# Kernel optimization log

Hardware: AMD Instinct MI355X
Metric: run time of the kernel (lower is better)

The kernel has to match this reference:

```python
import jax, jax.numpy as jnp
from jax import lax
import numpy as np

B, T, D = 8, 2048, 1024
EPS = 1e-8


def zc_rms(x, g):
    x0 = x - jnp.mean(x, axis=-1, keepdims=True)
    return x0 * jax.lax.rsqrt(jnp.mean(x0 * x0, axis=-1, keepdims=True) + EPS) * g


def l2norm(x):
    return x * jax.lax.rsqrt(jnp.sum(x * x, axis=-1, keepdims=True) + EPS)


def dwconv3(x, w, b):
    # x: [B, T, D]; w: [D, 3] depthwise kernel; b: [D]
    xc = jnp.transpose(x, (0, 2, 1))  # [B, D, T]
    y = lax.conv_general_dilated(xc, w[:, None, :], window_strides=(1,),
                                 padding=[(1, 1)],
                                 dimension_numbers=('NCH', 'OIH', 'NCH'),
                                 feature_group_count=w.shape[0])
    return jnp.transpose(y + b[:, None], (0, 2, 1))  # [B, T, D]


def setup_inputs() -> dict:
    key = jax.random.key(0)
    ks = jax.random.split(key, 16)
    s = 1.0 / np.sqrt(D)
    inp = {
        'x': jax.random.normal(ks[0], (B, T, D), jnp.float32),
        'g1': jnp.ones((D,), jnp.float32),
        'Wq': jax.random.normal(ks[1], (D, D), jnp.float32) * s,
        'bq': jnp.zeros((D,), jnp.float32),
        'Wk': jax.random.normal(ks[2], (D, D), jnp.float32) * s,
        'bk': jnp.zeros((D,), jnp.float32),
        'Wv': jax.random.normal(ks[3], (D, D), jnp.float32) * s,
        'bv': jnp.zeros((D,), jnp.float32),
        'wqc': jax.random.normal(ks[4], (D, 3), jnp.float32) * 0.5,
        'bqc': jnp.zeros((D,), jnp.float32),
        'wkc': jax.random.normal(ks[5], (D, 3), jnp.float32) * 0.5,
        'bkc': jnp.zeros((D,), jnp.float32),
        'wvc': jax.random.normal(ks[6], (D, 3), jnp.float32) * 0.5,
        'bvc': jnp.zeros((D,), jnp.float32),
        'Wa': jax.random.normal(ks[7], (D, D), jnp.float32) * s,
        'ba': jnp.zeros((D,), jnp.float32),
        'Wb': jax.random.normal(ks[8], (D, D), jnp.float32) * s,
        'bb': jnp.zeros((D,), jnp.float32),
        'g2': jnp.ones((D,), jnp.float32),
        'Wp': jax.random.normal(ks[9], (D, D), jnp.float32) * s,
        'bp': jnp.zeros((D,), jnp.float32),
    }
    return inp


def reference(x, g1, Wq, bq, Wk, bk, Wv, bv, wqc, bqc, wkc, bkc, wvc, bvc,
              Wa, ba, Wb, bb, g2, Wp, bp):
    h = zc_rms(x, g1)
    q = jax.nn.sigmoid(dwconv3(h @ Wq + bq, wqc, bqc))
    k = jax.nn.sigmoid(dwconv3(h @ Wk + bk, wkc, bkc))
    v = jax.nn.sigmoid(dwconv3(h @ Wv + bv, wvc, bvc))
    q, k = l2norm(q), l2norm(k)
    delta = q * (k * v)
    delta = jnp.tanh(x @ Wa + ba) * delta + (x @ Wb + bb)
    dhat = zc_rms(delta, g2) @ Wp + bp
    # dropout is identity in eval mode
    return x + jax.nn.sigmoid(jax.nn.silu(dhat)) * dhat
```

## Files before the change

### kernel.cpp

```cpp
#include <hip/hip_runtime.h>
#include <stdint.h>

#define DD 1024
#define TT 2048
#define BBATCH 8
#define MM (BBATCH*TT)

typedef unsigned short u16;
typedef unsigned int   u32;

typedef __attribute__((ext_vector_type(8))) __bf16 bf16x8;
typedef __attribute__((ext_vector_type(4))) float  floatx4;
typedef __attribute__((ext_vector_type(4))) unsigned short u16x4;
typedef __attribute__((ext_vector_type(8))) unsigned short u16x8;

__device__ __forceinline__ float b2f(u16 v){
    u32 x = ((u32)v) << 16;
    return __builtin_bit_cast(float, x);
}
__device__ __forceinline__ u16 f2b(float f){
    u32 u = __builtin_bit_cast(u32, f);
    u32 r = (u + 0x7fffu + ((u >> 16) & 1u)) >> 16;
    return (u16)r;
}
__device__ __forceinline__ float sigf(float x){
    return 1.0f / (1.0f + __expf(-x));
}
__device__ __forceinline__ float tanhfast(float x){
    float e = __expf(2.0f * x);
    return 1.0f - 2.0f / (e + 1.0f);
}

__device__ __forceinline__ void g2l16(const u16* g, u16* l){
    __builtin_amdgcn_global_load_lds(
        (const __attribute__((address_space(1))) u32*)g,
        (__attribute__((address_space(3))) u32*)l, 16, 0, 0);
}

__device__ __forceinline__ void load4bf(const u16* p, float* o){
    u16x4 v = *(const u16x4*)p;
    o[0] = b2f(v.x); o[1] = b2f(v.y); o[2] = b2f(v.z); o[3] = b2f(v.w);
}

__device__ __forceinline__ void wave_reduce2(float& a, float& b){
    #pragma unroll
    for (int m = 32; m; m >>= 1){
        a += __shfl_xor(a, m, 64);
        b += __shfl_xor(b, m, 64);
    }
}

__device__ __forceinline__ void block_reduce2(float& a, float& b, float* red, int tid){
    #pragma unroll
    for (int off = 32; off; off >>= 1){
        a += __shfl_down(a, off, 64);
        b += __shfl_down(b, off, 64);
    }
    __syncthreads();
    if ((tid & 63) == 0){ red[tid >> 6] = a; red[4 + (tid >> 6)] = b; }
    __syncthreads();
    a = red[0] + red[1] + red[2] + red[3];
    b = red[4] + red[5] + red[6] + red[7];
}

__global__ __launch_bounds__(256) void transpose_w(
    const float* __restrict__ s0, const float* __restrict__ s1, const float* __restrict__ s2,
    const float* __restrict__ s3, const float* __restrict__ s4, const float* __restrict__ s5,
    u16* __restrict__ dst_base)
{
    __shared__ u16 tile[32][33];
    const float* srcs[6] = {s0, s1, s2, s3, s4, s5};
    const int z = blockIdx.z;
    const float* src = srcs[z];
    u16* dst = dst_base + (size_t)z * (DD * (size_t)DD);
    const int tx = threadIdx.x, ty = threadIdx.y;
    const int x = blockIdx.x * 32 + tx;
    #pragma unroll
    for (int i = 0; i < 4; i++){
        int y = blockIdx.y * 32 + ty + i * 8;
        tile[ty + i * 8][tx] = f2b(src[(size_t)y * DD + x]);
    }
    __syncthreads();
    const int x2 = blockIdx.y * 32 + tx;
    #pragma unroll
    for (int i = 0; i < 4; i++){
        int y2 = blockIdx.x * 32 + ty + i * 8;
        dst[(size_t)y2 * DD + x2] = tile[tx][ty + i * 8];
    }
}

__global__ __launch_bounds__(256) void prep_wc(
    const float* __restrict__ w0, const float* __restrict__ w1, const float* __restrict__ w2,
    float* __restrict__ wcT)
{
    const float* srcs[3] = {w0, w1, w2};
    const int s = blockIdx.x / 3, tap = blockIdx.x % 3;
    #pragma unroll
    for (int i = 0; i < 4; i++){
        int d = threadIdx.x + i * 256;
        wcT[(s * 3 + tap) * DD + d] = srcs[s][d * 3 + tap];
    }
}

__global__ __launch_bounds__(256) void prep_rows(
    const float* __restrict__ in, const float* __restrict__ g,
    u16* __restrict__ xb, u16* __restrict__ h)
{
    const int tid = threadIdx.x;
    const int w = tid >> 6, lane = tid & 63;
    const int row = blockIdx.x * 4 + w;
    const int d0 = lane * 16;
    const size_t base = (size_t)row * DD + d0;

    float v[16];
    #pragma unroll
    for (int c = 0; c < 4; c++){
        floatx4 t = *(const floatx4*)(in + base + c * 4);
        v[c*4+0] = t.x; v[c*4+1] = t.y; v[c*4+2] = t.z; v[c*4+3] = t.w;
    }
    u16x8 x0, x1;
    #pragma unroll
    for (int j = 0; j < 8; j++){ x0[j] = f2b(v[j]); x1[j] = f2b(v[8+j]); }
    *(u16x8*)(xb + base)     = x0;
    *(u16x8*)(xb + base + 8) = x1;

    float s1 = 0.f, s2 = 0.f;
    #pragma unroll
    for (int j = 0; j < 16; j++){ s1 += v[j]; s2 += v[j]*v[j]; }
    wave_reduce2(s1, s2);
    const float mu = s1 * (1.0f / DD);
    const float ms = fmaxf(s2 * (1.0f / DD) - mu * mu, 0.0f);
    const float sc = rsqrtf(ms + 1e-8f);

    u16x8 o0, o1;
    #pragma unroll
    for (int j = 0; j < 8; j++)  o0[j] = f2b((v[j]     - mu) * sc * g[d0 + j]);
    #pragma unroll
    for (int j = 0; j < 8; j++)  o1[j] = f2b((v[8 + j] - mu) * sc * g[d0 + 8 + j]);
    *(u16x8*)(h + base)     = o0;
    *(u16x8*)(h + base + 8) = o1;
}

struct GemmPtrs {
    const u16*   A[5];
    const u16*   W[5];
    const float* bias[5];
    u16*         out[5];
};

template<int MODE>
__global__ __launch_bounds__(256) void gemm_bf16(
    GemmPtrs ptrs, const float* __restrict__ xres, float* __restrict__ dout)
{
    constexpr int BK = 32;
    __shared__ alignas(16) u16 As[128 * BK];
    __shared__ alignas(16) u16 Bs[128 * BK];

    const int z = blockIdx.z;
    const u16*   __restrict__ A    = ptrs.A[z];
    const u16*   __restrict__ W    = ptrs.W[z];
    const float* __restrict__ bias = ptrs.bias[z];
    u16* __restrict__ Cout = ptrs.out[z];

    const int tid  = threadIdx.x;
    const int wave = tid >> 6, lane = tid & 63;
    const int quad = lane >> 4, l16 = lane & 15;
    const int bm = blockIdx.x * 128;
    const int bn = blockIdx.y * 128;
    const int wm = (wave & 1) * 64, wn = (wave >> 1) * 64;

    const int c0 = tid, c1 = tid + 256;
    const int r0 = c0 >> 2, o0s = ((c0 & 3) ^ (r0 & 3)) * 8;
    const int r1 = c1 >> 2, o1s = ((c1 & 3) ^ (r1 & 3)) * 8;
    const u16* a0p = A + (size_t)(bm + r0) * DD + o0s;
    const u16* a1p = A + (size_t)(bm + r1) * DD + o1s;
    const u16* w0p = W + (size_t)(bn + r0) * DD + o0s;
    const u16* w1p = W + (size_t)(bn + r1) * DD + o1s;

    floatx4 acc[4][4];
    #pragma unroll
    for (int i = 0; i < 4; i++)
        #pragma unroll
        for (int j = 0; j < 4; j++)
            acc[i][j] = (floatx4){0.f, 0.f, 0.f, 0.f};

    for (int k0 = 0; k0 < DD; k0 += BK){
        g2l16(a0p + k0, &As[c0 * 8]);
        g2l16(a1p + k0, &As[c1 * 8]);
        g2l16(w0p + k0, &Bs[c0 * 8]);
        g2l16(w1p + k0, &Bs[c1 * 8]);
        __syncthreads();
        bf16x8 af[4], bfr[4];
        #pragma unroll
        for (int i = 0; i < 4; i++){
            int ra = wm + i * 16 + l16;
            int rb = wn + i * 16 + l16;
            af[i]  = *(const bf16x8*)&As[(ra * 4 + (quad ^ (ra & 3))) * 8];
            bfr[i] = *(const bf16x8*)&Bs[(rb * 4 + (quad ^ (rb & 3))) * 8];
        }
        #pragma unroll
        for (int i = 0; i < 4; i++)
            #pragma unroll
            for (int j = 0; j < 4; j++)
                acc[i][j] = __builtin_amdgcn_mfma_f32_16x16x32_bf16(af[i], bfr[j], acc[i][j], 0, 0, 0);
        __syncthreads();
    }

    float bj[4];
    #pragma unroll
    for (int j = 0; j < 4; j++) bj[j] = bias[bn + wn + j * 16 + l16];

    #pragma unroll
    for (int i = 0; i < 4; i++){
        const int rbase = bm + wm + i * 16 + quad * 4;
        #pragma unroll
        for (int j = 0; j < 4; j++){
            const int col = bn + wn + j * 16 + l16;
            #pragma unroll
            for (int r = 0; r < 4; r++){
                size_t idx = (size_t)(rbase + r) * DD + col;
                float zv = acc[i][j][r] + bj[j];
                if (MODE == 0){
                    Cout[idx] = f2b(zv);
                } else {
                    float sl = zv * sigf(zv);
                    dout[idx] = xres[idx] + sigf(sl) * zv;
                }
            }
        }
    }
}

__global__ __launch_bounds__(256) void mid_fuse(
    const u16* __restrict__ q0, const u16* __restrict__ k0, const u16* __restrict__ v0,
    const u16* __restrict__ a0, const u16* __restrict__ b0,
    const float* __restrict__ wcT,
    const float* __restrict__ bqc, const float* __restrict__ bkc, const float* __restrict__ bvc,
    const float* __restrict__ g2, u16* __restrict__ uout)
{
    __shared__ float red[8];
    const int row = blockIdx.x;
    const int t   = row & (TT - 1);
    const int tid = threadIdx.x;
    const int d0  = tid * 4;
    const size_t base = (size_t)row * DD + d0;
    const bool hm = (t > 0), hp = (t < TT - 1);

    float q[4], k[4], v[4];
    {
        const u16*   srcs[3] = {q0, k0, v0};
        const float* bs[3]   = {bqc, bkc, bvc};
        float* outs[3]       = {q, k, v};
        #pragma unroll
        for (int s = 0; s < 3; s++){
            float cm[4], cc[4], cp[4];
            load4bf(srcs[s] + base, cc);
            if (hm) load4bf(srcs[s] + base - DD, cm);
            else { cm[0]=0.f; cm[1]=0.f; cm[2]=0.f; cm[3]=0.f; }
            if (hp) load4bf(srcs[s] + base + DD, cp);
            else { cp[0]=0.f; cp[1]=0.f; cp[2]=0.f; cp[3]=0.f; }
            const float* wt = wcT + s * 3 * DD + d0;
            const float* bb = bs[s] + d0;
            #pragma unroll
            for (int j = 0; j < 4; j++){
                float y = cm[j] * wt[j] + cc[j] * wt[DD + j] + cp[j] * wt[2 * DD + j] + bb[j];
                outs[s][j] = sigf(y);
            }
        }
    }

    float sq = 0.f, sk = 0.f;
    #pragma unroll
    for (int j = 0; j < 4; j++){ sq += q[j] * q[j]; sk += k[j] * k[j]; }
    block_reduce2(sq, sk, red, tid);
    const float rq = rsqrtf(sq + 1e-8f), rk = rsqrtf(sk + 1e-8f);

    float av[4], bv[4];
    load4bf(a0 + base, av);
    load4bf(b0 + base, bv);

    float dl[4], s1 = 0.f, s2 = 0.f;
    #pragma unroll
    for (int j = 0; j < 4; j++){
        float d = (q[j] * rq) * (k[j] * rk) * v[j];
        d = tanhfast(av[j]) * d + bv[j];
        dl[j] = d; s1 += d; s2 += d * d;
    }
    block_reduce2(s1, s2, red, tid);
    const float mu = s1 * (1.0f / DD);
    const float ms = fmaxf(s2 * (1.0f / DD) - mu * mu, 0.0f);
    const float sc = rsqrtf(ms + 1e-8f);

    u16x4 ov;
    ov.x = f2b((dl[0] - mu) * sc * g2[d0 + 0]);
    ov.y = f2b((dl[1] - mu) * sc * g2[d0 + 1]);
    ov.z = f2b((dl[2] - mu) * sc * g2[d0 + 2]);
    ov.w = f2b((dl[3] - mu) * sc * g2[d0 + 3]);
    *(u16x4*)(uout + base) = ov;
}

extern "C" void kernel_launch(void* const* d_in, const int* in_sizes, int n_in,
                              void* d_out, int out_size, void* d_ws, size_t ws_size,
                              hipStream_t stream)
{
    const float* x   = (const float*)d_in[0];
    const float* g1  = (const float*)d_in[1];
    const float* Wq  = (const float*)d_in[2];
    const float* bq  = (const float*)d_in[3];
    const float* Wk  = (const float*)d_in[4];
    const float* bk  = (const float*)d_in[5];
    const float* Wv  = (const float*)d_in[6];
    const float* bv  = (const float*)d_in[7];
    const float* wqc = (const float*)d_in[8];
    const float* bqc = (const float*)d_in[9];
    const float* wkc = (const float*)d_in[10];
    const float* bkc = (const float*)d_in[11];
    const float* wvc = (const float*)d_in[12];
    const float* bvc = (const float*)d_in[13];
    const float* Wa  = (const float*)d_in[14];
    const float* ba  = (const float*)d_in[15];
    const float* Wb  = (const float*)d_in[16];
    const float* bb  = (const float*)d_in[17];
    const float* g2  = (const float*)d_in[18];
    const float* Wp  = (const float*)d_in[19];
    const float* bp  = (const float*)d_in[20];

    u16* ws = (u16*)d_ws;
    const size_t WSZ = (size_t)DD * DD;
    const size_t TSZ = (size_t)MM * DD;
    u16* WT = ws;
    float* wcT = (float*)(ws + 6 * WSZ);
    u16* xb = ws + 6 * WSZ + 32768;
    u16* h  = xb + TSZ;
    u16* q0 = h  + TSZ;
    u16* k0 = q0 + TSZ;
    u16* v0 = k0 + TSZ;
    u16* a0 = v0 + TSZ;
    u16* b0 = a0 + TSZ;
    u16* u  = h;

    transpose_w<<<dim3(32, 32, 6), dim3(32, 8, 1), 0, stream>>>(Wq, Wk, Wv, Wa, Wb, Wp, WT);
    prep_wc<<<dim3(9), dim3(256), 0, stream>>>(wqc, wkc, wvc, wcT);
    prep_rows<<<dim3(MM / 4), dim3(256), 0, stream>>>(x, g1, xb, h);

    GemmPtrs p0;
    p0.A[0] = h;  p0.W[0] = WT + 0 * WSZ; p0.bias[0] = bq; p0.out[0] = q0;
    p0.A[1] = h;  p0.W[1] = WT + 1 * WSZ; p0.bias[1] = bk; p0.out[1] = k0;
    p0.A[2] = h;  p0.W[2] = WT + 2 * WSZ; p0.bias[2] = bv; p0.out[2] = v0;
    p0.A[3] = xb; p0.W[3] = WT + 3 * WSZ; p0.bias[3] = ba; p0.out[3] = a0;
    p0.A[4] = xb; p0.W[4] = WT + 4 * WSZ; p0.bias[4] = bb; p0.out[4] = b0;
    gemm_bf16<0><<<dim3(128, 8, 5), dim3(256), 0, stream>>>(p0, nullptr, nullptr);

    mid_fuse<<<dim3(MM), dim3(256), 0, stream>>>(q0, k0, v0, a0, b0,
                                                 wcT, bqc, bkc, bvc, g2, u);

    GemmPtrs p1;
    for (int i = 0; i < 5; i++){ p1.A[i] = u; p1.W[i] = WT + 5 * WSZ; p1.bias[i] = bp; p1.out[i] = nullptr; }
    gemm_bf16<1><<<dim3(128, 8, 1), dim3(256), 0, stream>>>(p1, x, (float*)d_out);
}
```

Baseline: 516.1 us.

## Rewrite bf16 GEMM as 256x256 tiles with a 4-stage LDS pipeline

Each block now computes a 256x256 tile with 512 threads (8 waves), where each wave owns a 128x64 sub-tile. The K loop becomes a 4-buffer LDS pipeline: direct global-to-LDS copies run three tiles ahead, with explicit vmcnt waits and raw barriers, so memory traffic overlaps the MFMA work. The change also adds a rotated LDS swizzle, split fragment loads with intermediate barriers, and s_setprio around the MFMA bursts. The cost is a much larger LDS footprint (128KB) and higher register pressure, which limits occupancy. The final projection GEMM also drops to a single wave of 256 blocks.

```diff
diff --git a/kernel.cpp b/kernel.cpp
--- a/kernel.cpp
+++ b/kernel.cpp
@@ -148,13 +148,44 @@
     u16*         out[5];
 };
 
+__device__ __forceinline__ void tile_compute(
+    const u16* __restrict__ ab, const u16* __restrict__ bb,
+    const int (&aslot)[8], const int (&bslot)[4], floatx4 (&acc)[8][4])
+{
+    bf16x8 bfr[4], af[4];
+    #pragma unroll
+    for (int j = 0; j < 4; j++) bfr[j] = *(const bf16x8*)(bb + bslot[j]);
+    #pragma unroll
+    for (int i = 0; i < 4; i++) af[i] = *(const bf16x8*)(ab + aslot[i]);
+    __builtin_amdgcn_s_barrier();
+    asm volatile("" ::: "memory");
+    __builtin_amdgcn_s_setprio(1);
+    #pragma unroll
+    for (int i = 0; i < 4; i++)
+        #pragma unroll
+        for (int j = 0; j < 4; j++)
+            acc[i][j] = __builtin_amdgcn_mfma_f32_16x16x32_bf16(af[i], bfr[j], acc[i][j], 0, 0, 0);
+    __builtin_amdgcn_s_setprio(0);
+    #pragma unroll
+    for (int i = 0; i < 4; i++) af[i] = *(const bf16x8*)(ab + aslot[4 + i]);
+    __builtin_amdgcn_s_barrier();
+    asm volatile("" ::: "memory");
+    __builtin_amdgcn_s_setprio(1);
+    #pragma unroll
+    for (int i = 0; i < 4; i++)
+        #pragma unroll
+        for (int j = 0; j < 4; j++)
+            acc[4 + i][j] = __builtin_amdgcn_mfma_f32_16x16x32_bf16(af[i], bfr[j], acc[4 + i][j], 0, 0, 0);
+    __builtin_amdgcn_s_setprio(0);
+}
+
 template<int MODE>
-__global__ __launch_bounds__(256) void gemm_bf16(
+__global__ __launch_bounds__(512, 2) void gemm_bf16(
     GemmPtrs ptrs, const float* __restrict__ xres, float* __restrict__ dout)
 {
-    constexpr int BK = 32;
-    __shared__ alignas(16) u16 As[128 * BK];
-    __shared__ alignas(16) u16 Bs[128 * BK];
+    constexpr int NKT = DD / 32;
+    __shared__ alignas(16) u16 As[4][256 * 32];
+    __shared__ alignas(16) u16 Bs[4][256 * 32];
 
     const int z = blockIdx.z;
     const u16*   __restrict__ A    = ptrs.A[z];
@@ -165,57 +196,84 @@
     const int tid  = threadIdx.x;
     const int wave = tid >> 6, lane = tid & 63;
     const int quad = lane >> 4, l16 = lane & 15;
-    const int bm = blockIdx.x * 128;
-    const int bn = blockIdx.y * 128;
-    const int wm = (wave & 1) * 64, wn = (wave >> 1) * 64;
-
-    const int c0 = tid, c1 = tid + 256;
-    const int r0 = c0 >> 2, o0s = ((c0 & 3) ^ (r0 & 3)) * 8;
-    const int r1 = c1 >> 2, o1s = ((c1 & 3) ^ (r1 & 3)) * 8;
-    const u16* a0p = A + (size_t)(bm + r0) * DD + o0s;
-    const u16* a1p = A + (size_t)(bm + r1) * DD + o1s;
-    const u16* w0p = W + (size_t)(bn + r0) * DD + o0s;
-    const u16* w1p = W + (size_t)(bn + r1) * DD + o1s;
-
-    floatx4 acc[4][4];
-    #pragma unroll
-    for (int i = 0; i < 4; i++)
+    const int wrow = wave >> 2, wcol = wave & 3;
+    const int bm = blockIdx.x * 256;
+    const int bn = blockIdx.y * 256;
+
+    const int s0 = tid, s1 = tid + 512;
+    const int r0 = s0 >> 2, r1 = s1 >> 2;
+    const int o0 = (((s0 & 3) - r0 - (r0 >> 2)) & 3) * 8;
+    const int o1 = (((s1 & 3) - r1 - (r1 >> 2)) & 3) * 8;
+    const u16* a0p = A + (size_t)(bm + r0) * DD + o0;
+    const u16* a1p = A + (size_t)(bm + r1) * DD + o1;
+    const u16* w0p = W + (size_t)(bn + r0) * DD + o0;
+    const u16* w1p = W + (size_t)(bn + r1) * DD + o1;
+
+    #define STAGE(tt) do {                                   \
+        const int _b = (tt) & 3; const int _k = (tt) * 32;   \
+        g2l16(a0p + _k, &As[_b][s0 * 8]);                    \
+        g2l16(a1p + _k, &As[_b][s1 * 8]);                    \
+        g2l16(w0p + _k, &Bs[_b][s0 * 8]);                    \
+        g2l16(w1p + _k, &Bs[_b][s1 * 8]);                    \
+    } while (0)
+
+    STAGE(0); STAGE(1); STAGE(2);
+
+    int aslot[8], bslot[4];
+    #pragma unroll
+    for (int i = 0; i < 8; i++){
+        int rr = wrow * 128 + i * 16 + l16;
+        aslot[i] = (rr * 4 + ((quad + rr + (rr >> 2)) & 3)) * 8;
+    }
+    #pragma unroll
+    for (int j = 0; j < 4; j++){
+        int rr = wcol * 64 + j * 16 + l16;
+        bslot[j] = (rr * 4 + ((quad + rr + (rr >> 2)) & 3)) * 8;
+    }
+
+    floatx4 acc[8][4];
+    #pragma unroll
+    for (int i = 0; i < 8; i++)
         #pragma unroll
         for (int j = 0; j < 4; j++)
             acc[i][j] = (floatx4){0.f, 0.f, 0.f, 0.f};
 
-    for (int k0 = 0; k0 < DD; k0 += BK){
-        g2l16(a0p + k0, &As[c0 * 8]);
-        g2l16(a1p + k0, &As[c1 * 8]);
-        g2l16(w0p + k0, &Bs[c0 * 8]);
-        g2l16(w1p + k0, &Bs[c1 * 8]);
-        __syncthreads();
-        bf16x8 af[4], bfr[4];
-        #pragma unroll
-        for (int i = 0; i < 4; i++){
-            int ra = wm + i * 16 + l16;
-            int rb = wn + i * 16 + l16;
-            af[i]  = *(const bf16x8*)&As[(ra * 4 + (quad ^ (ra & 3))) * 8];
-            bfr[i] = *(const bf16x8*)&Bs[(rb * 4 + (quad ^ (rb & 3))) * 8];
-        }
-        #pragma unroll
-        for (int i = 0; i < 4; i++)
-            #pragma unroll
-            for (int j = 0; j < 4; j++)
-                acc[i][j] = __builtin_amdgcn_mfma_f32_16x16x32_bf16(af[i], bfr[j], acc[i][j], 0, 0, 0);
-        __syncthreads();
-    }
+    asm volatile("s_waitcnt vmcnt(8)" ::: "memory");
+    __builtin_amdgcn_s_barrier();
+    asm volatile("" ::: "memory");
+
+    int t = 0;
+    for (; t < NKT - 3; ++t){
+        STAGE(t + 3);
+        tile_compute(&As[t & 3][0], &Bs[t & 3][0], aslot, bslot, acc);
+        asm volatile("s_waitcnt vmcnt(8)" ::: "memory");
+        __builtin_amdgcn_s_barrier();
+        asm volatile("" ::: "memory");
+    }
+    tile_compute(&As[t & 3][0], &Bs[t & 3][0], aslot, bslot, acc);
+    asm volatile("s_waitcnt vmcnt(4)" ::: "memory");
+    __builtin_amdgcn_s_barrier();
+    asm volatile("" ::: "memory");
+    ++t;
+    tile_compute(&As[t & 3][0], &Bs[t & 3][0], aslot, bslot, acc);
+    asm volatile("s_waitcnt vmcnt(0)" ::: "memory");
+    __builtin_amdgcn_s_barrier();
+    asm volatile("" ::: "memory");
+    ++t;
+    tile_compute(&As[t & 3][0], &Bs[t & 3][0], aslot, bslot, acc);
+
+    #undef STAGE
 
     float bj[4];
     #pragma unroll
-    for (int j = 0; j < 4; j++) bj[j] = bias[bn + wn + j * 16 + l16];
-
-    #pragma unroll
-    for (int i = 0; i < 4; i++){
-        const int rbase = bm + wm + i * 16 + quad * 4;
+    for (int j = 0; j < 4; j++) bj[j] = bias[bn + wcol * 64 + j * 16 + l16];
+
+    #pragma unroll
+    for (int i = 0; i < 8; i++){
+        const int rbase = bm + wrow * 128 + i * 16 + quad * 4;
         #pragma unroll
         for (int j = 0; j < 4; j++){
-            const int col = bn + wn + j * 16 + l16;
+            const int col = bn + wcol * 64 + j * 16 + l16;
             #pragma unroll
             for (int r = 0; r < 4; r++){
                 size_t idx = (size_t)(rbase + r) * DD + col;
@@ -349,12 +407,12 @@
     p0.A[2] = h;  p0.W[2] = WT + 2 * WSZ; p0.bias[2] = bv; p0.out[2] = v0;
     p0.A[3] = xb; p0.W[3] = WT + 3 * WSZ; p0.bias[3] = ba; p0.out[3] = a0;
     p0.A[4] = xb; p0.W[4] = WT + 4 * WSZ; p0.bias[4] = bb; p0.out[4] = b0;
-    gemm_bf16<0><<<dim3(128, 8, 5), dim3(256), 0, stream>>>(p0, nullptr, nullptr);
+    gemm_bf16<0><<<dim3(64, 4, 5), dim3(512), 0, stream>>>(p0, nullptr, nullptr);
 
     mid_fuse<<<dim3(MM), dim3(256), 0, stream>>>(q0, k0, v0, a0, b0,
                                                  wcT, bqc, bkc, bvc, g2, u);
 
     GemmPtrs p1;
     for (int i = 0; i < 5; i++){ p1.A[i] = u; p1.W[i] = WT + 5 * WSZ; p1.bias[i] = bp; p1.out[i] = nullptr; }
-    gemm_bf16<1><<<dim3(128, 8, 1), dim3(256), 0, stream>>>(p1, x, (float*)d_out);
-}
+    gemm_bf16<1><<<dim3(64, 4, 1), dim3(512), 0, stream>>>(p1, x, (float*)d_out);
+}
```

Result: slower. 539.6 us (+4.6%).

## Rewrite GEMM as 256x256 tile, 8-wave, double-buffered pipelined MFMA kernel

Applied to the files above, without the earlier changes.

Replaces the 128x128, BK=32 single-buffered GEMM with a 256x256 tile, BK=64, 512-thread kernel. Global-to-LDS copies are double-buffered and interleaved with MFMA quadrants through manual s_barrier, waitcnt and setprio scheduling, with inline-asm ds_read_b128 loads on a swizzled layout. The aim is to hide load latency and raise data reuse per LDS byte. It uses 128KB of LDS per block, which limits occupancy. The hand-placed barriers and waitcnts risk races if they are wrong, and the larger tiles mean fewer blocks for the last GEMM.

```diff
diff --git a/kernel.cpp b/kernel.cpp
--- a/kernel.cpp
+++ b/kernel.cpp
@@ -13,6 +13,7 @@
 typedef __attribute__((ext_vector_type(4))) float  floatx4;
 typedef __attribute__((ext_vector_type(4))) unsigned short u16x4;
 typedef __attribute__((ext_vector_type(8))) unsigned short u16x8;
+typedef __attribute__((ext_vector_type(4))) unsigned int   u32x4;
 
 __device__ __forceinline__ float b2f(u16 v){
     u32 x = ((u32)v) << 16;
@@ -35,6 +36,30 @@
     __builtin_amdgcn_global_load_lds(
         (const __attribute__((address_space(1))) u32*)g,
         (__attribute__((address_space(3))) u32*)l, 16, 0, 0);
+}
+
+__device__ __forceinline__ u32 lds_u32(const u16* p){
+    return (u32)(size_t)(const __attribute__((address_space(3))) u16*)p;
+}
+
+template<int OFF>
+__device__ __forceinline__ bf16x8 dsr(u32 addr){
+    u32x4 d;
+    asm volatile("ds_read_b128 %0, %1 offset:%2" : "=v"(d) : "v"(addr), "i"(OFF));
+    return __builtin_bit_cast(bf16x8, d);
+}
+
+template<int BASE>
+__device__ __forceinline__ void rd_a8(bf16x8 (&arr)[8], u32 a){
+    arr[0]=dsr<BASE+0>(a);    arr[1]=dsr<BASE+64>(a);
+    arr[2]=dsr<BASE+2048>(a); arr[3]=dsr<BASE+2112>(a);
+    arr[4]=dsr<BASE+4096>(a); arr[5]=dsr<BASE+4160>(a);
+    arr[6]=dsr<BASE+6144>(a); arr[7]=dsr<BASE+6208>(a);
+}
+template<int BASE>
+__device__ __forceinline__ void rd_b4(bf16x8 (&arr)[4], u32 a){
+    arr[0]=dsr<BASE+0>(a);    arr[1]=dsr<BASE+64>(a);
+    arr[2]=dsr<BASE+2048>(a); arr[3]=dsr<BASE+2112>(a);
 }
 
 __device__ __forceinline__ void load4bf(const u16* p, float* o){
@@ -148,13 +173,30 @@
     u16*         out[5];
 };
 
+#define BAR()   asm volatile("s_barrier" ::: "memory")
+#define LGKM0() asm volatile("s_waitcnt lgkmcnt(0)" ::: "memory")
+#define VM8()   asm volatile("s_waitcnt vmcnt(8)" ::: "memory")
+#define SB0()   __builtin_amdgcn_sched_barrier(0)
+#define PRIO1() __builtin_amdgcn_s_setprio(1)
+#define PRIO0() __builtin_amdgcn_s_setprio(0)
+
+template<int IH, int JH>
+__device__ __forceinline__ void mm8(floatx4 (&acc)[8][4], const bf16x8 (&af)[8], const bf16x8 (&bf)[4]){
+    #pragma unroll
+    for (int kk = 0; kk < 2; kk++)
+        #pragma unroll
+        for (int i = 0; i < 4; i++)
+            #pragma unroll
+            for (int j = 0; j < 2; j++)
+                acc[IH*4+i][JH*2+j] = __builtin_amdgcn_mfma_f32_16x16x32_bf16(
+                    af[i*2+kk], bf[j*2+kk], acc[IH*4+i][JH*2+j], 0, 0, 0);
+}
+
 template<int MODE>
-__global__ __launch_bounds__(256) void gemm_bf16(
+__global__ __launch_bounds__(512, 2) void gemm_bf16(
     GemmPtrs ptrs, const float* __restrict__ xres, float* __restrict__ dout)
 {
-    constexpr int BK = 32;
-    __shared__ alignas(16) u16 As[128 * BK];
-    __shared__ alignas(16) u16 Bs[128 * BK];
+    __shared__ alignas(16) u16 lds[65536];
 
     const int z = blockIdx.z;
     const u16*   __restrict__ A    = ptrs.A[z];
@@ -165,60 +207,79 @@
     const int tid  = threadIdx.x;
     const int wave = tid >> 6, lane = tid & 63;
     const int quad = lane >> 4, l16 = lane & 15;
-    const int bm = blockIdx.x * 128;
-    const int bn = blockIdx.y * 128;
-    const int wm = (wave & 1) * 64, wn = (wave >> 1) * 64;
-
-    const int c0 = tid, c1 = tid + 256;
-    const int r0 = c0 >> 2, o0s = ((c0 & 3) ^ (r0 & 3)) * 8;
-    const int r1 = c1 >> 2, o1s = ((c1 & 3) ^ (r1 & 3)) * 8;
-    const u16* a0p = A + (size_t)(bm + r0) * DD + o0s;
-    const u16* a1p = A + (size_t)(bm + r1) * DD + o1s;
-    const u16* w0p = W + (size_t)(bn + r0) * DD + o0s;
-    const u16* w1p = W + (size_t)(bn + r1) * DD + o1s;
-
-    floatx4 acc[4][4];
-    #pragma unroll
-    for (int i = 0; i < 4; i++)
+    const int wrow = wave >> 2, wcol = wave & 3;
+    const int bm = blockIdx.x * 256;
+    const int bn = blockIdx.y * 256;
+
+    const int coloff = ((tid & 7) * 8) ^ (((tid >> 5) & 1) << 4);
+    const u16* srcA = A + (size_t)(bm + (tid >> 3)) * DD + coloff;
+    const u16* srcB = W + (size_t)(bn + (tid >> 3)) * DD + coloff;
+
+    #define STAGE_A(T,H) do{ \
+        u16* _d = &lds[(((T)&1)*2 + (H))*8192 + tid*8]; \
+        const u16* _g = srcA + (size_t)(H)*128*DD + (size_t)(((T)&15)*64); \
+        g2l16(_g, _d); g2l16(_g + (size_t)64*DD, _d + 4096); }while(0)
+    #define STAGE_B(T,H) do{ \
+        u16* _d = &lds[32768 + (((T)&1)*2 + (H))*8192 + tid*8]; \
+        const u16* _g = srcB + (size_t)(H)*128*DD + (size_t)(((T)&15)*64); \
+        g2l16(_g, _d); g2l16(_g + (size_t)64*DD, _d + 4096); }while(0)
+
+    const u32 swz = (u32)((quad * 16) ^ (((l16 >> 2) & 1) << 5));
+    const u32 lbase = lds_u32(&lds[0]);
+    u32 addr_a = lbase + (u32)(wrow * 8192 + l16 * 128) + swz;
+    u32 addr_b = lbase + 65536u + (u32)(wcol * 4096 + l16 * 128) + swz;
+
+    floatx4 acc[8][4];
+    #pragma unroll
+    for (int i = 0; i < 8; i++)
         #pragma unroll
         for (int j = 0; j < 4; j++)
             acc[i][j] = (floatx4){0.f, 0.f, 0.f, 0.f};
 
-    for (int k0 = 0; k0 < DD; k0 += BK){
-        g2l16(a0p + k0, &As[c0 * 8]);
-        g2l16(a1p + k0, &As[c1 * 8]);
-        g2l16(w0p + k0, &Bs[c0 * 8]);
-        g2l16(w1p + k0, &Bs[c1 * 8]);
-        __syncthreads();
-        bf16x8 af[4], bfr[4];
-        #pragma unroll
-        for (int i = 0; i < 4; i++){
-            int ra = wm + i * 16 + l16;
-            int rb = wn + i * 16 + l16;
-            af[i]  = *(const bf16x8*)&As[(ra * 4 + (quad ^ (ra & 3))) * 8];
-            bfr[i] = *(const bf16x8*)&Bs[(rb * 4 + (quad ^ (rb & 3))) * 8];
-        }
-        #pragma unroll
-        for (int i = 0; i < 4; i++)
-            #pragma unroll
-            for (int j = 0; j < 4; j++)
-                acc[i][j] = __builtin_amdgcn_mfma_f32_16x16x32_bf16(af[i], bfr[j], acc[i][j], 0, 0, 0);
-        __syncthreads();
-    }
+    STAGE_A(0,0); STAGE_B(0,0); STAGE_B(0,1); STAGE_A(0,1); STAGE_A(1,0); STAGE_B(1,0);
+    VM8(); BAR();
+
+    bf16x8 af0[8], af1[8], bf0[4], bf1[4];
+
+    for (int t = 0; t < 16; ++t){
+        rd_a8<0>(af0, addr_a);
+        rd_b4<0>(bf0, addr_b);
+        STAGE_B(t+1, 1);
+        BAR(); LGKM0(); SB0();
+        PRIO1(); mm8<0,0>(acc, af0, bf0); PRIO0(); SB0();
+        VM8(); BAR();
+        rd_b4<16384>(bf1, addr_b);
+        STAGE_A(t+1, 1);
+        BAR(); LGKM0(); SB0();
+        PRIO1(); mm8<0,1>(acc, af0, bf1); PRIO0(); SB0();
+        VM8(); BAR();
+        rd_a8<16384>(af1, addr_a);
+        STAGE_A(t+2, 0);
+        BAR(); LGKM0(); SB0();
+        PRIO1(); mm8<1,0>(acc, af1, bf0); PRIO0(); SB0();
+        STAGE_B(t+2, 0);
+        PRIO1(); mm8<1,1>(acc, af1, bf1); PRIO0(); SB0();
+        VM8(); BAR();
+        addr_a ^= 32768u; addr_b ^= 32768u;
+    }
+
+    #undef STAGE_A
+    #undef STAGE_B
 
     float bj[4];
     #pragma unroll
-    for (int j = 0; j < 4; j++) bj[j] = bias[bn + wn + j * 16 + l16];
-
-    #pragma unroll
-    for (int i = 0; i < 4; i++){
-        const int rbase = bm + wm + i * 16 + quad * 4;
+    for (int j = 0; j < 4; j++)
+        bj[j] = bias[bn + (j >= 2 ? 128 : 0) + wcol * 32 + (j & 1) * 16 + l16];
+
+    #pragma unroll
+    for (int i = 0; i < 8; i++){
+        const int row0 = bm + (i >= 4 ? 128 : 0) + wrow * 64 + (i & 3) * 16 + quad * 4;
         #pragma unroll
         for (int j = 0; j < 4; j++){
-            const int col = bn + wn + j * 16 + l16;
+            const int col = bn + (j >= 2 ? 128 : 0) + wcol * 32 + (j & 1) * 16 + l16;
             #pragma unroll
             for (int r = 0; r < 4; r++){
-                size_t idx = (size_t)(rbase + r) * DD + col;
+                size_t idx = (size_t)(row0 + r) * DD + col;
                 float zv = acc[i][j][r] + bj[j];
                 if (MODE == 0){
                     Cout[idx] = f2b(zv);
@@ -349,12 +410,12 @@
     p0.A[2] = h;  p0.W[2] = WT + 2 * WSZ; p0.bias[2] = bv; p0.out[2] = v0;
     p0.A[3] = xb; p0.W[3] = WT + 3 * WSZ; p0.bias[3] = ba; p0.out[3] = a0;
     p0.A[4] = xb; p0.W[4] = WT + 4 * WSZ; p0.bias[4] = bb; p0.out[4] = b0;
-    gemm_bf16<0><<<dim3(128, 8, 5), dim3(256), 0, stream>>>(p0, nullptr, nullptr);
+    gemm_bf16<0><<<dim3(64, 4, 5), dim3(512), 0, stream>>>(p0, nullptr, nullptr);
 
     mid_fuse<<<dim3(MM), dim3(256), 0, stream>>>(q0, k0, v0, a0, b0,
                                                  wcT, bqc, bkc, bvc, g2, u);
 
     GemmPtrs p1;
     for (int i = 0; i < 5; i++){ p1.A[i] = u; p1.W[i] = WT + 5 * WSZ; p1.bias[i] = bp; p1.out[i] = nullptr; }
-    gemm_bf16<1><<<dim3(128, 8, 1), dim3(256), 0, stream>>>(p1, x, (float*)d_out);
-}
+    gemm_bf16<1><<<dim3(64, 4, 1), dim3(512), 0, stream>>>(p1, x, (float*)d_out);
+}
```

After: 470.3 us. 8.9% less time.
